# Kernel tuning notes

Hardware: AMD Instinct MI355X
Metric: run time of the kernel (lower is better)

Reference implementation:

```python
import jax, jax.numpy as jnp
import numpy as np

D_LOB = 128
D_HAWKES = 32
N_HEADS = 4
HEAD_DIM = D_LOB // N_HEADS
LN_EPS = 1e-5


def setup_inputs() -> dict:
    key = jax.random.key(0)
    ks = jax.random.split(key, 10)
    B, T = 8, 2048
    s = lambda fan_in: 1.0 / np.sqrt(fan_in)
    return {
        "lob": jax.random.normal(ks[0], (B, T, D_LOB), dtype=jnp.float32),
        "hawkes": jax.random.normal(ks[1], (B, T, D_HAWKES), dtype=jnp.float32),
        # hawkes_proj: Linear(d_hawkes, d_lob)
        "Wp": jax.random.uniform(ks[2], (D_LOB, D_HAWKES), jnp.float32, -s(D_HAWKES), s(D_HAWKES)),
        "bp": jnp.zeros((D_LOB,), jnp.float32),
        # MultiheadAttention packed in-projection (3*d_lob, d_lob) and out-projection
        "Win": jax.random.uniform(ks[3], (3 * D_LOB, D_LOB), jnp.float32, -s(D_LOB), s(D_LOB)),
        "bin_": jnp.zeros((3 * D_LOB,), jnp.float32),
        "Wo": jax.random.uniform(ks[4], (D_LOB, D_LOB), jnp.float32, -s(D_LOB), s(D_LOB)),
        "bo": jnp.zeros((D_LOB,), jnp.float32),
        # LayerNorm affine params
        "gamma": jnp.ones((D_LOB,), jnp.float32),
        "beta": jnp.zeros((D_LOB,), jnp.float32),
    }


def reference(lob, hawkes, Wp, bp, Win, bin_, Wo, bo, gamma, beta):
    B, T, _ = lob.shape
    # hawkes_proj
    h = hawkes @ Wp.T + bp  # (B, T, d_lob)
    # packed QKV projection (query=lob, key=value=h)
    q = lob @ Win[:D_LOB].T + bin_[:D_LOB]
    k = h @ Win[D_LOB:2 * D_LOB].T + bin_[D_LOB:2 * D_LOB]
    v = h @ Win[2 * D_LOB:].T + bin_[2 * D_LOB:]
    # split heads -> (B, H, T, hd)
    split = lambda x: x.reshape(B, T, N_HEADS, HEAD_DIM).transpose(0, 2, 1, 3)
    q, k, v = split(q), split(k), split(v)
    scale = 1.0 / np.sqrt(HEAD_DIM).astype(np.float32)
    scores = jnp.einsum("bhqd,bhkd->bhqk", q * scale, k)  # (B, H, T, T)
    attn = jax.nn.softmax(scores, axis=-1)
    # dropout(p=0.1) omitted: reference is eval/inference mode
    ctx = jnp.einsum("bhqk,bhkd->bhqd", attn, v)  # (B, H, T, hd)
    ctx = ctx.transpose(0, 2, 1, 3).reshape(B, T, D_LOB)
    fused = ctx @ Wo.T + bo
    # residual + LayerNorm
    x = lob + fused
    mu = jnp.mean(x, axis=-1, keepdims=True)
    var = jnp.mean(jnp.square(x - mu), axis=-1, keepdims=True)
    out = (x - mu) * jax.lax.rsqrt(var + LN_EPS) * gamma + beta
    attn_w = jnp.mean(attn, axis=1)  # average over heads (B, T, T)
    return out, attn_w
```

## Files before the change

kernel.cpp:

```cpp
#include <hip/hip_runtime.h>
#include <hip/hip_bf16.h>
#include <math.h>

#define TT 2048
#define BB 8
#define DD 128
#define HH 4
#define BT (BB*TT)
#define BH (BB*HH)
#define SCALE 0.1767766952966369f
#define S2LOG (SCALE * 1.4426950408889634f)

typedef __attribute__((ext_vector_type(8))) short short8;
typedef __attribute__((ext_vector_type(4))) short short4v;
typedef __attribute__((ext_vector_type(4))) float f32x4;
typedef __hip_bfloat16 bf16;

#define MFMA16(a,b,c) __builtin_amdgcn_mfma_f32_16x16x32_bf16(a,b,c,0,0,0)

static __device__ inline short8 ldg8(const bf16* p) {
  return *reinterpret_cast<const short8*>(p);
}
static __device__ inline short4v ldg4(const bf16* p) {
  return *reinterpret_cast<const short4v*>(p);
}
static __device__ inline short f2bs(float x) {
  bf16 h = __float2bfloat16(x);
  return *reinterpret_cast<short*>(&h);
}
static __device__ inline short fpack(float x) {
  unsigned u = *reinterpret_cast<unsigned*>(&x);
  return (short)((u + 0x8000u) >> 16);
}
static __device__ inline short8 ldcvt8(const float* p) {
  f32x4 f0 = *reinterpret_cast<const f32x4*>(p);
  f32x4 f1 = *reinterpret_cast<const f32x4*>(p + 4);
  short8 r;
  #pragma unroll
  for (int i = 0; i < 4; ++i) { r[i] = f2bs(f0[i]); r[4+i] = f2bs(f1[i]); }
  return r;
}

__global__ __launch_bounds__(256) void proj_kernel(
    const float* __restrict__ lob, const float* __restrict__ hawkes,
    const float* __restrict__ Wp, const float* __restrict__ bp,
    const float* __restrict__ Win, const float* __restrict__ binp,
    bf16* __restrict__ qg, bf16* __restrict__ kg, bf16* __restrict__ vtg) {
  __shared__ bf16 hT[32*136];
  __shared__ bf16 sK[32*136];
  __shared__ bf16 vT[128*40];
  int tid = threadIdx.x;
  int wave = tid >> 6, lane = tid & 63;
  int lr = lane & 15, lq = lane >> 4;
  int r0 = blockIdx.x * 32;
  int b  = r0 >> 11, t0 = r0 & 2047;
  f32x4 z = {0.f,0.f,0.f,0.f};

  short8 alob[2][4], ahk[2];
  #pragma unroll
  for (int mt = 0; mt < 2; ++mt) {
    const float* lp = lob + (size_t)(r0 + mt*16 + lr)*128;
    #pragma unroll
    for (int kt = 0; kt < 4; ++kt) alob[mt][kt] = ldcvt8(lp + kt*32 + lq*8);
    ahk[mt] = ldcvt8(hawkes + (size_t)(r0 + mt*16 + lr)*32 + lq*8);
  }

  for (int nt = wave; nt < 8; nt += 4) {
    int cn = nt*16;
    short8 bfrag = ldcvt8(Wp + (size_t)(cn + lr)*32 + lq*8);
    float bias = bp[cn + lr];
    #pragma unroll
    for (int mt = 0; mt < 2; ++mt) {
      f32x4 c = MFMA16(ahk[mt], bfrag, z);
      #pragma unroll
      for (int r = 0; r < 4; ++r)
        hT[(mt*16 + lq*4 + r)*136 + cn + lr] = __float2bfloat16(c[r] + bias);
    }
  }
  __syncthreads();

  short8 ah[2][4];
  #pragma unroll
  for (int mt = 0; mt < 2; ++mt)
    #pragma unroll
    for (int kt = 0; kt < 4; ++kt)
      ah[mt][kt] = *reinterpret_cast<const short8*>(&hT[(mt*16 + lr)*136 + kt*32 + lq*8]);
  __syncthreads();

  for (int nt = wave; nt < 24; nt += 4) {
    int which = nt >> 3;
    int c = (nt & 7)*16 + lr;
    const float* wrow = Win + (size_t)(which*128 + c)*128;
    float bias = binp[which*128 + c];
    f32x4 acc0 = z, acc1 = z;
    #pragma unroll
    for (int kt = 0; kt < 4; ++kt) {
      short8 bfrag = ldcvt8(wrow + kt*32 + lq*8);
      if (which == 0) {
        acc0 = MFMA16(alob[0][kt], bfrag, acc0);
        acc1 = MFMA16(alob[1][kt], bfrag, acc1);
      } else {
        acc0 = MFMA16(ah[0][kt], bfrag, acc0);
        acc1 = MFMA16(ah[1][kt], bfrag, acc1);
      }
    }
    #pragma unroll
    for (int mt = 0; mt < 2; ++mt) {
      f32x4 acc = mt ? acc1 : acc0;
      #pragma unroll
      for (int r = 0; r < 4; ++r) {
        int row = mt*16 + lq*4 + r;
        float val = acc[r] + bias;
        if (which == 0)      hT[row*136 + c] = __float2bfloat16(val);
        else if (which == 1) sK[row*136 + c] = __float2bfloat16(val);
        else                 vT[c*40 + row]  = __float2bfloat16(val);
      }
    }
  }
  __syncthreads();

  {
    int head = tid >> 6, tt = (tid >> 1) & 31, half = tid & 1;
    const bf16* sq = &hT[tt*136 + head*32 + half*16];
    const bf16* sk = &sK[tt*136 + head*32 + half*16];
    bf16* qdst = qg + ((size_t)(b*HH + head)*TT + t0 + tt)*32 + half*16;
    bf16* kdst = kg + ((size_t)(b*HH + head)*TT + t0 + tt)*32 + half*16;
    *reinterpret_cast<short8*>(qdst)     = *reinterpret_cast<const short8*>(sq);
    *reinterpret_cast<short8*>(qdst + 8) = *reinterpret_cast<const short8*>(sq + 8);
    *reinterpret_cast<short8*>(kdst)     = *reinterpret_cast<const short8*>(sk);
    *reinterpret_cast<short8*>(kdst + 8) = *reinterpret_cast<const short8*>(sk + 8);
  }
  {
    int dd = tid >> 1, half = tid & 1;
    int bh = b*HH + (dd >> 5);
    short8 s0 = *reinterpret_cast<const short8*>(&vT[dd*40 + half*16]);
    short8 s1 = *reinterpret_cast<const short8*>(&vT[dd*40 + half*16 + 8]);
    bf16* dst = vtg + ((size_t)bh*32 + (dd & 31))*TT + t0 + half*16;
    *reinterpret_cast<short8*>(dst) = s0;
    *reinterpret_cast<short8*>(dst + 8) = s1;
  }
}

__global__ __launch_bounds__(256) void attn_kernel(const bf16* __restrict__ qg,
    const bf16* __restrict__ kg, const bf16* __restrict__ vtg,
    float* __restrict__ attn_out, bf16* __restrict__ ctxg) {
  int wgid = (blockIdx.x & 7)*64 + (blockIdx.x >> 3);
  int b = wgid >> 6, qt = wgid & 63;
  int tid = threadIdx.x;
  int head = tid >> 6, lane = tid & 63;
  int lr = lane & 15, lq = lane >> 4;
  int bh = b*HH + head;
  __shared__ float plds[2][4][32*36];
  const bf16* qp = qg + ((size_t)bh*TT + (size_t)qt*32)*32;
  const bf16* kb = kg + (size_t)bh*TT*32;
  const bf16* vb = vtg + (size_t)bh*32*TT;
  f32x4 z = {0.f,0.f,0.f,0.f};

  short8 aq0 = ldg8(qp + lr*32 + lq*8);
  short8 aq1 = ldg8(qp + (16+lr)*32 + lq*8);

  float rs0 = 0.f, rs1 = 0.f;
  {
    short8 kA0 = ldg8(kb + (size_t)lr*32 + lq*8);
    short8 kA1 = ldg8(kb + (size_t)(16+lr)*32 + lq*8);
    short8 kB0, kB1;
#define P1STEP(KC0, KC1, KN0, KN1, NCC) { \
    int nc_ = (NCC); \
    KN0 = ldg8(kb + (size_t)(nc_*32 + lr)*32 + lq*8); \
    KN1 = ldg8(kb + (size_t)(nc_*32 + 16 + lr)*32 + lq*8); \
    f32x4 sa0 = MFMA16(KC0, aq0, z), sb0 = MFMA16(KC1, aq0, z); \
    f32x4 sa1 = MFMA16(KC0, aq1, z), sb1 = MFMA16(KC1, aq1, z); \
    _Pragma("unroll") for (int r = 0; r < 4; ++r) { \
      rs0 += exp2f(sa0[r]*S2LOG) + exp2f(sb0[r]*S2LOG); \
      rs1 += exp2f(sa1[r]*S2LOG) + exp2f(sb1[r]*S2LOG); } }
    #pragma unroll 1
    for (int c = 0; c < 64; c += 2) {
      P1STEP(kA0, kA1, kB0, kB1, c+1);
      P1STEP(kB0, kB1, kA0, kA1, (c+2 < 64) ? c+2 : 0);
    }
#undef P1STEP
  }
  rs0 += __shfl_xor(rs0, 16, 64); rs0 += __shfl_xor(rs0, 32, 64);
  rs1 += __shfl_xor(rs1, 16, 64); rs1 += __shfl_xor(rs1, 32, 64);
  float lb0 = -log2f(rs0);
  float lb1 = -log2f(rs1);

  f32x4 acc00 = z, acc01 = z, acc10 = z, acc11 = z;
  float* awr = attn_out + (size_t)(b*TT + qt*32)*TT;
  int mq = tid >> 3, mk = (tid & 7)*4;

  short8 kA0 = ldg8(kb + (size_t)lr*32 + lq*8);
  short8 kA1 = ldg8(kb + (size_t)(16+lr)*32 + lq*8);
  short4v vA00 = ldg4(vb + (size_t)lr*TT + lq*4);
  short4v vA01 = ldg4(vb + (size_t)lr*TT + 16 + lq*4);
  short4v vA10 = ldg4(vb + (size_t)(16+lr)*TT + lq*4);
  short4v vA11 = ldg4(vb + (size_t)(16+lr)*TT + 16 + lq*4);
  short8 kB0, kB1; short4v vB00, vB01, vB10, vB11;

#define P2STEP(KC, KC0, KC1, VC00, VC01, VC10, VC11, KN0, KN1, VN00, VN01, VN10, VN11, NCC) { \
    int kc_ = (KC); int nc_ = (NCC); int pb_ = kc_ & 1; \
    KN0 = ldg8(kb + (size_t)(nc_*32 + lr)*32 + lq*8); \
    KN1 = ldg8(kb + (size_t)(nc_*32 + 16 + lr)*32 + lq*8); \
    VN00 = ldg4(vb + (size_t)lr*TT + nc_*32 + lq*4); \
    VN01 = ldg4(vb + (size_t)lr*TT + nc_*32 + 16 + lq*4); \
    VN10 = ldg4(vb + (size_t)(16+lr)*TT + nc_*32 + lq*4); \
    VN11 = ldg4(vb + (size_t)(16+lr)*TT + nc_*32 + 16 + lq*4); \
    f32x4 s00 = MFMA16(KC0, aq0, z), s10 = MFMA16(KC1, aq0, z); \
    f32x4 s01 = MFMA16(KC0, aq1, z), s11 = MFMA16(KC1, aq1, z); \
    f32x4 p00, p10, p01, p11; \
    _Pragma("unroll") for (int r = 0; r < 4; ++r) { \
      p00[r] = exp2f(fmaf(s00[r], S2LOG, lb0)); \
      p10[r] = exp2f(fmaf(s10[r], S2LOG, lb0)); \
      p01[r] = exp2f(fmaf(s01[r], S2LOG, lb1)); \
      p11[r] = exp2f(fmaf(s11[r], S2LOG, lb1)); } \
    { float* pw = &plds[pb_][head][0]; \
      *reinterpret_cast<f32x4*>(pw + lr*36 + lq*4)           = p00; \
      *reinterpret_cast<f32x4*>(pw + lr*36 + 16 + lq*4)      = p10; \
      *reinterpret_cast<f32x4*>(pw + (16+lr)*36 + lq*4)      = p01; \
      *reinterpret_cast<f32x4*>(pw + (16+lr)*36 + 16 + lq*4) = p11; } \
    short8 ap0, ap1; \
    _Pragma("unroll") for (int r = 0; r < 4; ++r) { \
      ap0[r] = fpack(p00[r]); ap0[4+r] = fpack(p10[r]); \
      ap1[r] = fpack(p01[r]); ap1[4+r] = fpack(p11[r]); } \
    __syncthreads(); \
    { const float* pr = &plds[pb_][0][0]; \
      f32x4 mv = *reinterpret_cast<const f32x4*>(pr + mq*36 + mk); \
      mv = mv + *reinterpret_cast<const f32x4*>(pr + 1152 + mq*36 + mk); \
      mv = mv + *reinterpret_cast<const f32x4*>(pr + 2304 + mq*36 + mk); \
      mv = mv + *reinterpret_cast<const f32x4*>(pr + 3456 + mq*36 + mk); \
      *reinterpret_cast<f32x4*>(awr + (size_t)mq*TT + kc_*32 + mk) = mv * 0.25f; } \
    short8 vf0, vf1; \
    _Pragma("unroll") for (int j = 0; j < 4; ++j) { \
      vf0[j] = VC00[j]; vf0[4+j] = VC01[j]; \
      vf1[j] = VC10[j]; vf1[4+j] = VC11[j]; } \
    acc00 = MFMA16(ap0, vf0, acc00); acc01 = MFMA16(ap0, vf1, acc01); \
    acc10 = MFMA16(ap1, vf0, acc10); acc11 = MFMA16(ap1, vf1, acc11); }

  #pragma unroll 1
  for (int c = 0; c < 64; c += 2) {
    P2STEP(c,   kA0, kA1, vA00, vA01, vA10, vA11,
                kB0, kB1, vB00, vB01, vB10, vB11, c+1);
    P2STEP(c+1, kB0, kB1, vB00, vB01, vB10, vB11,
                kA0, kA1, vA00, vA01, vA10, vA11, (c+2 < 64) ? c+2 : 0);
  }
#undef P2STEP

  __syncthreads();
  float* sX = &plds[0][0][0];
  #pragma unroll
  for (int m = 0; m < 2; ++m) {
    f32x4 a0 = m ? acc10 : acc00;
    f32x4 a1 = m ? acc11 : acc01;
    #pragma unroll
    for (int r = 0; r < 4; ++r) {
      int row = m*16 + lq*4 + r;
      sX[row*132 + head*32 + lr]      = a0[r];
      sX[row*132 + head*32 + 16 + lr] = a1[r];
    }
  }
  __syncthreads();
  {
    int q = tid >> 3, d0 = (tid & 7)*16;
    const float* xp = &sX[q*132 + d0];
    f32x4 x0 = *reinterpret_cast<const f32x4*>(xp);
    f32x4 x1 = *reinterpret_cast<const f32x4*>(xp + 4);
    f32x4 x2 = *reinterpret_cast<const f32x4*>(xp + 8);
    f32x4 x3 = *reinterpret_cast<const f32x4*>(xp + 12);
    short8 o0, o1;
    #pragma unroll
    for (int j = 0; j < 4; ++j) {
      o0[j] = f2bs(x0[j]); o0[4+j] = f2bs(x1[j]);
      o1[j] = f2bs(x2[j]); o1[4+j] = f2bs(x3[j]);
    }
    bf16* dst = ctxg + (size_t)(b*TT + qt*32 + q)*128 + d0;
    *reinterpret_cast<short8*>(dst)     = o0;
    *reinterpret_cast<short8*>(dst + 8) = o1;
  }
}

__global__ __launch_bounds__(256) void outln_kernel(const bf16* __restrict__ ctxg,
    const float* __restrict__ lob, const float* __restrict__ Wo,
    const float* __restrict__ bo, const float* __restrict__ gamma,
    const float* __restrict__ beta, float* __restrict__ outg) {
  __shared__ float sX[32*132];
  __shared__ float sPar[256];
  int tid = threadIdx.x, wave = tid >> 6, lane = tid & 63;
  int lr = lane & 15, lq = lane >> 4;
  int r0 = blockIdx.x * 32;
  if (tid < 128) { sPar[tid] = gamma[tid]; sPar[128+tid] = beta[tid]; }
  f32x4 z = {0.f,0.f,0.f,0.f};
  short8 actx[2][4];
  #pragma unroll
  for (int mt = 0; mt < 2; ++mt)
    #pragma unroll
    for (int kt = 0; kt < 4; ++kt)
      actx[mt][kt] = ldg8(ctxg + (size_t)(r0 + mt*16 + lr)*128 + kt*32 + lq*8);
  for (int nt = wave; nt < 8; nt += 4) {
    f32x4 acc0 = z, acc1 = z;
    #pragma unroll
    for (int kt = 0; kt < 4; ++kt) {
      short8 bfrag = ldcvt8(Wo + (size_t)(nt*16 + lr)*128 + kt*32 + lq*8);
      acc0 = MFMA16(actx[0][kt], bfrag, acc0);
      acc1 = MFMA16(actx[1][kt], bfrag, acc1);
    }
    int d = nt*16 + lr;
    float bias = bo[d];
    #pragma unroll
    for (int mt = 0; mt < 2; ++mt) {
      f32x4 acc = mt ? acc1 : acc0;
      #pragma unroll
      for (int r = 0; r < 4; ++r) {
        int row = mt*16 + lq*4 + r;
        sX[row*132 + d] = acc[r] + bias + lob[(size_t)(r0 + row)*128 + d];
      }
    }
  }
  __syncthreads();
  {
    int row = tid >> 3, j = tid & 7;
    const float* xp = &sX[row*132 + j*16];
    f32x4 x[4];
    #pragma unroll
    for (int v = 0; v < 4; ++v) x[v] = *reinterpret_cast<const f32x4*>(xp + v*4);
    float sum = 0.f, sq = 0.f;
    #pragma unroll
    for (int v = 0; v < 4; ++v)
      #pragma unroll
      for (int e = 0; e < 4; ++e) { sum += x[v][e]; sq += x[v][e]*x[v][e]; }
    #pragma unroll
    for (int mdx = 1; mdx < 8; mdx <<= 1) {
      sum += __shfl_xor(sum, mdx, 64);
      sq  += __shfl_xor(sq,  mdx, 64);
    }
    float mu = sum * (1.0f/128.0f);
    float rstd = rsqrtf(sq*(1.0f/128.0f) - mu*mu + 1e-5f);
    float* op = outg + (size_t)(r0 + row)*128 + j*16;
    #pragma unroll
    for (int v = 0; v < 4; ++v) {
      f32x4 o;
      #pragma unroll
      for (int e = 0; e < 4; ++e) {
        int d = j*16 + v*4 + e;
        o[e] = (x[v][e] - mu)*rstd*sPar[d] + sPar[128+d];
      }
      *reinterpret_cast<f32x4*>(op + v*4) = o;
    }
  }
}

extern "C" void kernel_launch(void* const* d_in, const int* in_sizes, int n_in,
                              void* d_out, int out_size, void* d_ws, size_t ws_size,
                              hipStream_t stream) {
  const float* lob    = (const float*)d_in[0];
  const float* hawkes = (const float*)d_in[1];
  const float* Wp     = (const float*)d_in[2];
  const float* bp     = (const float*)d_in[3];
  const float* Win    = (const float*)d_in[4];
  const float* binp   = (const float*)d_in[5];
  const float* Wo     = (const float*)d_in[6];
  const float* bo     = (const float*)d_in[7];
  const float* gamma  = (const float*)d_in[8];
  const float* beta   = (const float*)d_in[9];
  float* outg = (float*)d_out;
  float* attn_out = outg + (size_t)BT*128;

  char* ws = (char*)d_ws;
  bf16*  qg   = (bf16*)(ws);
  bf16*  kg   = (bf16*)(ws + (size_t)4*1024*1024);
  bf16*  vtg  = (bf16*)(ws + (size_t)8*1024*1024);
  bf16*  ctxg = (bf16*)(ws + (size_t)12*1024*1024);

  proj_kernel<<<BT/32, 256, 0, stream>>>(lob, hawkes, Wp, bp, Win, binp, qg, kg, vtg);
  attn_kernel<<<BB*(TT/32), 256, 0, stream>>>(qg, kg, vtg, attn_out, ctxg);
  outln_kernel<<<512, 256, 0, stream>>>(ctxg, lob, Wo, bo, gamma, beta, outg);
}
```

Measured before the change: 283.5 us.

## Fuse out-projection and LayerNorm into attention kernel epilogue; use packed bf16 convert

```diff
diff --git a/kernel.cpp b/kernel.cpp
--- a/kernel.cpp
+++ b/kernel.cpp
@@ -14,6 +14,7 @@
 typedef __attribute__((ext_vector_type(8))) short short8;
 typedef __attribute__((ext_vector_type(4))) short short4v;
 typedef __attribute__((ext_vector_type(4))) float f32x4;
+typedef __attribute__((ext_vector_type(4))) unsigned u32x4;
 typedef __hip_bfloat16 bf16;
 
 #define MFMA16(a,b,c) __builtin_amdgcn_mfma_f32_16x16x32_bf16(a,b,c,0,0,0)
@@ -28,9 +29,10 @@
   bf16 h = __float2bfloat16(x);
   return *reinterpret_cast<short*>(&h);
 }
-static __device__ inline short fpack(float x) {
-  unsigned u = *reinterpret_cast<unsigned*>(&x);
-  return (short)((u + 0x8000u) >> 16);
+static __device__ inline unsigned cvtpk(float lo, float hi) {
+  unsigned r;
+  asm("v_cvt_pk_bf16_f32 %0, %1, %2" : "=v"(r) : "v"(lo), "v"(hi));
+  return r;
 }
 static __device__ inline short8 ldcvt8(const float* p) {
   f32x4 f0 = *reinterpret_cast<const f32x4*>(p);
@@ -143,7 +145,10 @@
 
 __global__ __launch_bounds__(256) void attn_kernel(const bf16* __restrict__ qg,
     const bf16* __restrict__ kg, const bf16* __restrict__ vtg,
-    float* __restrict__ attn_out, bf16* __restrict__ ctxg) {
+    float* __restrict__ attn_out, const float* __restrict__ lobf,
+    const float* __restrict__ Wo, const float* __restrict__ bo,
+    const float* __restrict__ gamma, const float* __restrict__ beta,
+    float* __restrict__ outg) {
   int wgid = (blockIdx.x & 7)*64 + (blockIdx.x >> 3);
   int b = wgid >> 6, qt = wgid & 63;
   int tid = threadIdx.x;
@@ -218,10 +223,13 @@
       *reinterpret_cast<f32x4*>(pw + lr*36 + 16 + lq*4)      = p10; \
       *reinterpret_cast<f32x4*>(pw + (16+lr)*36 + lq*4)      = p01; \
       *reinterpret_cast<f32x4*>(pw + (16+lr)*36 + 16 + lq*4) = p11; } \
-    short8 ap0, ap1; \
-    _Pragma("unroll") for (int r = 0; r < 4; ++r) { \
-      ap0[r] = fpack(p00[r]); ap0[4+r] = fpack(p10[r]); \
-      ap1[r] = fpack(p01[r]); ap1[4+r] = fpack(p11[r]); } \
+    u32x4 ua_, ub_; \
+    ua_[0] = cvtpk(p00[0], p00[1]); ua_[1] = cvtpk(p00[2], p00[3]); \
+    ua_[2] = cvtpk(p10[0], p10[1]); ua_[3] = cvtpk(p10[2], p10[3]); \
+    ub_[0] = cvtpk(p01[0], p01[1]); ub_[1] = cvtpk(p01[2], p01[3]); \
+    ub_[2] = cvtpk(p11[0], p11[1]); ub_[3] = cvtpk(p11[2], p11[3]); \
+    short8 ap0 = *reinterpret_cast<short8*>(&ua_); \
+    short8 ap1 = *reinterpret_cast<short8*>(&ub_); \
     __syncthreads(); \
     { const float* pr = &plds[pb_][0][0]; \
       f32x4 mv = *reinterpret_cast<const f32x4*>(pr + mq*36 + mk); \
@@ -246,7 +254,9 @@
 #undef P2STEP
 
   __syncthreads();
-  float* sX = &plds[0][0][0];
+  size_t rowbase = (size_t)(b*TT) + (size_t)qt*32;
+  float* sX  = &plds[0][0][0];
+  float* sX2 = &plds[1][0][0];
   #pragma unroll
   for (int m = 0; m < 2; ++m) {
     f32x4 a0 = m ? acc10 : acc00;
@@ -259,43 +269,20 @@
     }
   }
   __syncthreads();
-  {
-    int q = tid >> 3, d0 = (tid & 7)*16;
-    const float* xp = &sX[q*132 + d0];
-    f32x4 x0 = *reinterpret_cast<const f32x4*>(xp);
-    f32x4 x1 = *reinterpret_cast<const f32x4*>(xp + 4);
-    f32x4 x2 = *reinterpret_cast<const f32x4*>(xp + 8);
-    f32x4 x3 = *reinterpret_cast<const f32x4*>(xp + 12);
-    short8 o0, o1;
-    #pragma unroll
-    for (int j = 0; j < 4; ++j) {
-      o0[j] = f2bs(x0[j]); o0[4+j] = f2bs(x1[j]);
-      o1[j] = f2bs(x2[j]); o1[4+j] = f2bs(x3[j]);
-    }
-    bf16* dst = ctxg + (size_t)(b*TT + qt*32 + q)*128 + d0;
-    *reinterpret_cast<short8*>(dst)     = o0;
-    *reinterpret_cast<short8*>(dst + 8) = o1;
-  }
-}
-
-__global__ __launch_bounds__(256) void outln_kernel(const bf16* __restrict__ ctxg,
-    const float* __restrict__ lob, const float* __restrict__ Wo,
-    const float* __restrict__ bo, const float* __restrict__ gamma,
-    const float* __restrict__ beta, float* __restrict__ outg) {
-  __shared__ float sX[32*132];
-  __shared__ float sPar[256];
-  int tid = threadIdx.x, wave = tid >> 6, lane = tid & 63;
-  int lr = lane & 15, lq = lane >> 4;
-  int r0 = blockIdx.x * 32;
-  if (tid < 128) { sPar[tid] = gamma[tid]; sPar[128+tid] = beta[tid]; }
-  f32x4 z = {0.f,0.f,0.f,0.f};
   short8 actx[2][4];
   #pragma unroll
   for (int mt = 0; mt < 2; ++mt)
     #pragma unroll
-    for (int kt = 0; kt < 4; ++kt)
-      actx[mt][kt] = ldg8(ctxg + (size_t)(r0 + mt*16 + lr)*128 + kt*32 + lq*8);
-  for (int nt = wave; nt < 8; nt += 4) {
+    for (int kt = 0; kt < 4; ++kt) {
+      const float* cp = &sX[(mt*16 + lr)*132 + kt*32 + lq*8];
+      f32x4 c0 = *reinterpret_cast<const f32x4*>(cp);
+      f32x4 c1 = *reinterpret_cast<const f32x4*>(cp + 4);
+      u32x4 u;
+      u[0] = cvtpk(c0[0], c0[1]); u[1] = cvtpk(c0[2], c0[3]);
+      u[2] = cvtpk(c1[0], c1[1]); u[3] = cvtpk(c1[2], c1[3]);
+      actx[mt][kt] = *reinterpret_cast<short8*>(&u);
+    }
+  for (int nt = head; nt < 8; nt += 4) {
     f32x4 acc0 = z, acc1 = z;
     #pragma unroll
     for (int kt = 0; kt < 4; ++kt) {
@@ -311,14 +298,14 @@
       #pragma unroll
       for (int r = 0; r < 4; ++r) {
         int row = mt*16 + lq*4 + r;
-        sX[row*132 + d] = acc[r] + bias + lob[(size_t)(r0 + row)*128 + d];
+        sX2[row*132 + d] = acc[r] + bias + lobf[(rowbase + row)*128 + d];
       }
     }
   }
   __syncthreads();
   {
     int row = tid >> 3, j = tid & 7;
-    const float* xp = &sX[row*132 + j*16];
+    const float* xp = &sX2[row*132 + j*16];
     f32x4 x[4];
     #pragma unroll
     for (int v = 0; v < 4; ++v) x[v] = *reinterpret_cast<const f32x4*>(xp + v*4);
@@ -334,14 +321,14 @@
     }
     float mu = sum * (1.0f/128.0f);
     float rstd = rsqrtf(sq*(1.0f/128.0f) - mu*mu + 1e-5f);
-    float* op = outg + (size_t)(r0 + row)*128 + j*16;
+    float* op = outg + (rowbase + row)*128 + j*16;
     #pragma unroll
     for (int v = 0; v < 4; ++v) {
       f32x4 o;
       #pragma unroll
       for (int e = 0; e < 4; ++e) {
         int d = j*16 + v*4 + e;
-        o[e] = (x[v][e] - mu)*rstd*sPar[d] + sPar[128+d];
+        o[e] = (x[v][e] - mu)*rstd*gamma[d] + beta[d];
       }
       *reinterpret_cast<f32x4*>(op + v*4) = o;
     }
@@ -368,9 +355,8 @@
   bf16*  qg   = (bf16*)(ws);
   bf16*  kg   = (bf16*)(ws + (size_t)4*1024*1024);
   bf16*  vtg  = (bf16*)(ws + (size_t)8*1024*1024);
-  bf16*  ctxg = (bf16*)(ws + (size_t)12*1024*1024);
 
   proj_kernel<<<BT/32, 256, 0, stream>>>(lob, hawkes, Wp, bp, Win, binp, qg, kg, vtg);
-  attn_kernel<<<BB*(TT/32), 256, 0, stream>>>(qg, kg, vtg, attn_out, ctxg);
-  outln_kernel<<<512, 256, 0, stream>>>(ctxg, lob, Wo, bo, gamma, beta, outg);
-}
+  attn_kernel<<<BB*(TT/32), 256, 0, stream>>>(qg, kg, vtg, attn_out,
+                                              lob, Wo, bo, gamma, beta, outg);
+}
```

After: 278.4 us. No clear change (-1.8%).
